# Performance work log

Hardware: AMD Instinct MI355X
Metric: run time of the kernel (lower is better)

The kernel has to match this reference:

```python
import jax, jax.numpy as jnp
import numpy as np
from jax import lax

B, N, E = 256, 100_000, 3_200_000
VOCAB, EMB, FT, DIM, OUT = 65, 128, 41, 32, 128
BN_EPS = 1e-5


def setup_inputs() -> dict:
    key = jax.random.key(0)
    ks = jax.random.split(key, 40)
    f = lambda i, shape: jax.random.normal(ks[i], shape, jnp.float32) * 0.05
    inp = {
        'xd': jax.random.randint(ks[0], (B, 100), 0, VOCAB),
        'xt': jax.random.normal(ks[1], (N, FT), jnp.float32),
        'edge_index': jax.random.randint(ks[2], (2, E), 0, N),
        'batch': jnp.sort(jax.random.randint(ks[3], (N,), 0, B)),
        'y': jax.random.normal(ks[4], (B,), jnp.float32),
        # drug branch params
        'emb': f(5, (VOCAB, EMB)),
        'conv_w': f(6, (32, 100, 8)),   # OIH for Conv1d(100->32, k=8)
        'conv_b': f(7, (32,)),
        'fcd_w': f(8, (32 * 121, OUT)),
        'fcd_b': f(9, (OUT,)),
        # GIN layer 1 MLP (41->32->32)
        'g1_w1': f(10, (FT, DIM)), 'g1_b1': f(11, (DIM,)),
        'g1_w2': f(12, (DIM, DIM)), 'g1_b2': f(13, (DIM,)),
        # GIN layers 2-5 MLPs (32->32->32), stacked
        'gw1': f(14, (4, DIM, DIM)), 'gb1': f(15, (4, DIM)),
        'gw2': f(16, (4, DIM, DIM)), 'gb2': f(17, (4, DIM)),
        # BatchNorm (eval mode running stats) for 5 layers
        'bn_g': f(18, (5, DIM)) + 1.0,
        'bn_b': f(19, (5, DIM)),
        'bn_rm': f(20, (5, DIM)),
        'bn_rv': jax.random.uniform(ks[21], (5, DIM), jnp.float32, 0.5, 1.5),
        # protein fc + classifier
        'fct_w': f(22, (DIM, OUT)), 'fct_b': f(23, (OUT,)),
        'c1_w': f(24, (256, 1024)), 'c1_b': f(25, (1024,)),
        'c2_w': f(26, (1024, 256)), 'c2_b': f(27, (256,)),
        'c3_w': f(28, (256, 1)), 'c3_b': f(29, (1,)),
    }
    return inp


def reference(xd, xt, edge_index, batch, y, emb, conv_w, conv_b, fcd_w, fcd_b,
              g1_w1, g1_b1, g1_w2, g1_b2, gw1, gb1, gw2, gb2,
              bn_g, bn_b, bn_rm, bn_rv, fct_w, fct_b,
              c1_w, c1_b, c2_w, c2_b, c3_w, c3_b):
    # ---- drug branch ----
    e = emb[xd]                                        # [B, 100, 128]
    c = lax.conv_general_dilated(e, conv_w, (1,), 'VALID',
                                 dimension_numbers=('NCH', 'OIH', 'NCH'))
    c = c + conv_b[None, :, None]                      # [B, 32, 121]
    xd_f = c.reshape(B, 32 * 121) @ fcd_w + fcd_b      # [B, 128]

    src, dst = edge_index[0], edge_index[1]
    h = xt
    for i in range(5):
        agg = h + jax.ops.segment_sum(h[src], dst, num_segments=N)
        if i == 0:
            w1, b1, w2, b2 = g1_w1, g1_b1, g1_w2, g1_b2
        else:
            w1, b1, w2, b2 = gw1[i - 1], gb1[i - 1], gw2[i - 1], gb2[i - 1]
        h = jax.nn.relu(agg @ w1 + b1) @ w2 + b2       # GIN MLP
        h = jax.nn.relu(h)                              # F.relu after conv
        h = bn_g[i] * (h - bn_rm[i]) * lax.rsqrt(bn_rv[i] + BN_EPS) + bn_b[i]
    pooled = jax.ops.segment_sum(h, batch, num_segments=B)  # global_add_pool
    xt_f = jax.nn.relu(pooled @ fct_w + fct_b)         # dropout = identity (eval)

    # ---- classifier ----
    xj = jnp.concatenate([xd_f, xt_f], axis=1)         # [B, 256]
    h1 = jax.nn.relu(xj @ c1_w + c1_b)
    h2 = jax.nn.relu(h1 @ c2_w + c2_b)
    out = (h2 @ c3_w + c3_b).squeeze(1)                # [B]
    return out, y
```

## Files before the change

### kernel.cpp

```cpp
#include <hip/hip_runtime.h>

typedef unsigned int u32;
typedef unsigned char u8;

#define NN 100000
#define NE 3200000
#define NB 256
#define FTD 41
#define DIM 32
#define NBK 782
#define SCHUNK 8000

typedef __fp16 fp16x2 __attribute__((ext_vector_type(2)));

__device__ __forceinline__ float h16f(u32 bits) {
  union { unsigned short s; _Float16 h; } c;
  c.s = (unsigned short)bits;
  return (float)c.h;
}
__device__ __forceinline__ u32 pk2(float a, float b) {
  union { fp16x2 h; u32 u; } c;
  c.h = __builtin_amdgcn_cvt_pkrtz(a, b);
  return c.u;
}

__device__ __forceinline__ u8 f8enc(float v) {
  union { _Float16 h; unsigned short u; } cv;
  cv.h = (_Float16)(v * 0.00390625f);
  u32 h = cv.u;
  u32 mag = h & 0x7fffu;
  u32 base = mag >> 7;
  u32 low = mag & 0x7fu;
  base += (low > 0x40u || (low == 0x40u && (base & 1u))) ? 1u : 0u;
  if (base > 0x7eu) base = 0x7eu;
  return (u8)(((h >> 8) & 0x80u) | base);
}

__device__ __forceinline__ void acc4(u32 w, float* a) {
#pragma unroll
  for (int i = 0; i < 4; i++) {
    u32 bb = (w >> (8 * i)) & 0xffu;
    a[i] += h16f(((bb & 0x80u) << 8) | ((bb & 0x7fu) << 7));
  }
}
__device__ __forceinline__ void accrow(uint4 r0, uint4 r1, float* acc) {
  acc4(r0.x, acc + 0);  acc4(r0.y, acc + 4);
  acc4(r0.z, acc + 8);  acc4(r0.w, acc + 12);
  acc4(r1.x, acc + 16); acc4(r1.y, acc + 20);
  acc4(r1.z, acc + 24); acc4(r1.w, acc + 28);
}

__global__ __launch_bounds__(256) void k_bzero(int* __restrict__ bcnt) {
  int g = blockIdx.x * 256 + threadIdx.x;
  if (g < NBK) bcnt[g] = 0;
}

__global__ __launch_bounds__(256) void k_bhist(const int* __restrict__ ei,
                                               int* __restrict__ bcnt) {
  __shared__ int h[NBK];
  int t = threadIdx.x;
  for (int i = t; i < NBK; i += 256) h[i] = 0;
  __syncthreads();
  for (int g = blockIdx.x * 256 + t; g < NE; g += gridDim.x * 256)
    atomicAdd(&h[ei[NE + g] >> 7], 1);
  __syncthreads();
  for (int i = t; i < NBK; i += 256)
    if (h[i]) atomicAdd(&bcnt[i], h[i]);
}

__global__ __launch_bounds__(1024) void k_bscan(const int* __restrict__ bcnt,
                                                int* __restrict__ boff,
                                                int* __restrict__ bcur) {
  __shared__ int sm[1024];
  int t = threadIdx.x;
  int v = (t < NBK) ? bcnt[t] : 0;
  sm[t] = v;
  __syncthreads();
  for (int d = 1; d < 1024; d <<= 1) {
    int x = (t >= d) ? sm[t - d] : 0;
    __syncthreads();
    sm[t] += x;
    __syncthreads();
  }
  if (t < NBK) {
    int excl = sm[t] - v;
    boff[t] = excl;
    bcur[t] = excl;
  }
  if (t == 0) boff[NBK] = NE;
}

__global__ __launch_bounds__(256) void k_bscatter(const int* __restrict__ ei,
                                                  int* __restrict__ bcur,
                                                  int* __restrict__ ppack) {
  __shared__ int lexcl[NBK];
  __shared__ int lcur[NBK];
  __shared__ int gdelta[NBK];
  __shared__ int lbuf[SCHUNK];
  __shared__ unsigned short lbkt[SCHUNK];
  __shared__ int sm[256];
  int t = threadIdx.x;
  int e0 = blockIdx.x * SCHUNK;
  for (int i = t; i < NBK; i += 256) lexcl[i] = 0;
  __syncthreads();
  for (int i = t; i < SCHUNK; i += 256)
    atomicAdd(&lexcl[((u32)ei[NE + e0 + i]) >> 7], 1);
  __syncthreads();
  int b0 = t * 4;
  int c0 = 0, c1 = 0, c2 = 0, c3 = 0;
  if (b0 < NBK) {
    c0 = lexcl[b0];
    c1 = (b0 + 1 < NBK) ? lexcl[b0 + 1] : 0;
    c2 = (b0 + 2 < NBK) ? lexcl[b0 + 2] : 0;
    c3 = (b0 + 3 < NBK) ? lexcl[b0 + 3] : 0;
  }
  int tot = c0 + c1 + c2 + c3;
  sm[t] = tot;
  __syncthreads();
  for (int d = 1; d < 256; d <<= 1) {
    int x = (t >= d) ? sm[t - d] : 0;
    __syncthreads();
    sm[t] += x;
    __syncthreads();
  }
  int base = sm[t] - tot;
  if (b0 < NBK) {
    int cnts[4] = {c0, c1, c2, c3};
    int e = base;
#pragma unroll
    for (int j = 0; j < 4; j++) {
      int b = b0 + j;
      if (b < NBK) {
        int c = cnts[j];
        lexcl[b] = e;
        lcur[b] = e;
        if (c > 0) gdelta[b] = atomicAdd(&bcur[b], c) - e;
        e += c;
      }
    }
  }
  __syncthreads();
  for (int i = t; i < SCHUNK; i += 256) {
    int s = ei[e0 + i];
    u32 d = (u32)ei[NE + e0 + i];
    int b = d >> 7;
    int p = atomicAdd(&lcur[b], 1);
    lbuf[p] = (int)(((d & 127u) << 20) | (u32)s);
    lbkt[p] = (unsigned short)b;
  }
  __syncthreads();
  for (int i = t; i < SCHUNK; i += 256) {
    int b = lbkt[i];
    ppack[gdelta[b] + i] = lbuf[i];
  }
}

__global__ __launch_bounds__(256) void k_bfinal(const int* __restrict__ boff,
                                                const int* __restrict__ ppack,
                                                int* __restrict__ off,
                                                int* __restrict__ srcs) {
  __shared__ int ncnt[128];
  __shared__ int nincl[128];
  int b = blockIdx.x, t = threadIdx.x;
  int e0 = boff[b], e1 = boff[b + 1];
  if (t < 128) ncnt[t] = 0;
  __syncthreads();
  for (int i = e0 + t; i < e1; i += 256) atomicAdd(&ncnt[((u32)ppack[i]) >> 20], 1);
  __syncthreads();
  if (t < 128) nincl[t] = ncnt[t];
  __syncthreads();
  for (int d = 1; d < 128; d <<= 1) {
    int x = 0;
    if (t < 128 && t >= d) x = nincl[t - d];
    __syncthreads();
    if (t < 128) nincl[t] += x;
    __syncthreads();
  }
  int node0 = b * 128;
  if (t < 128) {
    int excl = nincl[t] - ncnt[t];
    int node = node0 + t;
    if (node < NN) off[node] = e0 + excl;
    ncnt[t] = excl;
  }
  if (b == 0 && t == 0) off[NN] = NE;
  __syncthreads();
  for (int i = e0 + t; i < e1; i += 256) {
    u32 v = (u32)ppack[i];
    int dl = v >> 20;
    int pos = atomicAdd(&ncnt[dl], 1);
    srcs[e0 + pos] = (int)(v & 0xFFFFF);
  }
}

__global__ __launch_bounds__(256) void k_conv(
    const int* __restrict__ xd, const float* __restrict__ emb,
    const float* __restrict__ convw, const float* __restrict__ convb,
    float* __restrict__ C) {
  __shared__ float e_s[100 * 129 + 12];
  __shared__ float w_s[4 * 800];
  __shared__ int xd_s[100];
  int t = threadIdx.x;
  int b = blockIdx.x >> 3;
  int og = (blockIdx.x & 7) << 2;
  if (t < 100) xd_s[t] = xd[b * 100 + t];
  __syncthreads();
  for (int i = t; i < 12800; i += 256)
    e_s[(i >> 7) * 129 + (i & 127)] = emb[xd_s[i >> 7] * 128 + (i & 127)];
  for (int i = t; i < 3200; i += 256) w_s[i] = convw[og * 800 + i];
  __syncthreads();
  int ol = t >> 6;
  int ht = t & 63;
  int h0 = ht * 2;
  float a0 = 0.f, a1 = 0.f;
  const float4* wv = (const float4*)&w_s[ol * 800];
  for (int i = 0; i < 100; i++) {
    const float* ep = &e_s[i * 129 + h0];
    float e0 = ep[0], e1 = ep[1], e2 = ep[2], e3 = ep[3], e4 = ep[4];
    float e5 = ep[5], e6 = ep[6], e7 = ep[7], e8 = ep[8];
    float4 wa = wv[i * 2], wb = wv[i * 2 + 1];
    a0 += e0 * wa.x + e1 * wa.y + e2 * wa.z + e3 * wa.w +
          e4 * wb.x + e5 * wb.y + e6 * wb.z + e7 * wb.w;
    a1 += e1 * wa.x + e2 * wa.y + e3 * wa.z + e4 * wa.w +
          e5 * wb.x + e6 * wb.y + e7 * wb.z + e8 * wb.w;
  }
  int o = og + ol;
  float bb = convb[o];
  float* cp = &C[b * 3872 + o * 121];
  if (h0 < 121) cp[h0] = a0 + bb;
  if (h0 + 1 < 121) cp[h0 + 1] = a1 + bb;
}

__global__ __launch_bounds__(256) void k_fcd(
    const float* __restrict__ C, const float* __restrict__ fcdw,
    const float* __restrict__ fcdb, float* __restrict__ XJ) {
  __shared__ float c_s[3872];
  __shared__ float red[128];
  int t = threadIdx.x, b = blockIdx.x;
  for (int i = t; i < 3872; i += 256) c_s[i] = C[b * 3872 + i];
  __syncthreads();
  int j = t & 127, half = t >> 7;
  float acc = 0.f;
  int k0 = half * 1936;
  for (int k = k0; k < k0 + 1936; k++) acc += c_s[k] * fcdw[k * 128 + j];
  if (half) red[j] = acc;
  __syncthreads();
  if (!half) XJ[b * 256 + j] = acc + red[j] + fcdb[j];
}

__global__ __launch_bounds__(256) void k_z1(
    const float* __restrict__ xt, const float* __restrict__ w1,
    u8* __restrict__ Z, float* __restrict__ pool) {
  __shared__ float xs[256 * FTD];
  __shared__ float w1s[FTD * DIM];
  int t = threadIdx.x;
  int base = blockIdx.x * 256;
  int g = base + t;
  if (g < NB * DIM) pool[g] = 0.f;
  for (int i = t; i < FTD * DIM; i += 256) w1s[i] = w1[i];
  int cnt = min(256, NN - base);
  for (int i = t; i < cnt * FTD; i += 256) xs[i] = xt[base * FTD + i];
  __syncthreads();
  int n = base + t;
  if (n < NN) {
    float acc[DIM];
#pragma unroll
    for (int j = 0; j < DIM; j++) acc[j] = 0.f;
    for (int k = 0; k < FTD; k++) {
      float xk = xs[t * FTD + k];
#pragma unroll
      for (int j = 0; j < DIM; j++) acc[j] += xk * w1s[k * DIM + j];
    }
    u8* zp = &Z[n * DIM];
#pragma unroll
    for (int j = 0; j < DIM; j++) zp[j] = f8enc(acc[j]);
  }
}

template <int HAS_NEXT, int DO_POOL>
__global__ __launch_bounds__(256) void k_gin(
    const int* __restrict__ off, const int* __restrict__ srcs,
    const u8* __restrict__ Zin, const float* __restrict__ b1,
    const float* __restrict__ w2, const float* __restrict__ b2,
    const float* __restrict__ bng, const float* __restrict__ bnb,
    const float* __restrict__ bnrm, const float* __restrict__ bnrv,
    const float* __restrict__ w1n, u8* __restrict__ Zout,
    float* __restrict__ pool, const int* __restrict__ batch) {
  __shared__ float w2s[DIM * DIM];
  __shared__ float w1ns[DIM * DIM];
  __shared__ u32 aggs[256 * 17];
  int t = threadIdx.x;
  for (int i = t; i < DIM * DIM; i += 256) {
    w2s[i] = w2[i];
    if (HAS_NEXT) w1ns[i] = w1n[i];
  }
  int m = t >> 2, p = t & 3;
  int n = blockIdx.x * 64 + m;
  if (n < NN) {
    float acc[DIM];
#pragma unroll
    for (int i = 0; i < DIM; i++) acc[i] = 0.f;
    int beg = off[n], end = off[n + 1];
    if (p == 0) {
      const uint4* zr = (const uint4*)(Zin + n * DIM);
      uint4 r0 = zr[0], r1 = zr[1];
      accrow(r0, r1, acc);
    }
    int j = beg + p;
    for (; j + 4 < end; j += 8) {
      int sA = srcs[j], sB = srcs[j + 4];
      const uint4* ra = (const uint4*)(Zin + sA * DIM);
      const uint4* rb = (const uint4*)(Zin + sB * DIM);
      uint4 a0 = ra[0], a1 = ra[1];
      uint4 c0 = rb[0], c1 = rb[1];
      accrow(a0, a1, acc);
      accrow(c0, c1, acc);
    }
    if (j < end) {
      int sA = srcs[j];
      const uint4* ra = (const uint4*)(Zin + sA * DIM);
      uint4 a0 = ra[0], a1 = ra[1];
      accrow(a0, a1, acc);
    }
#pragma unroll
    for (int q = 0; q < 16; q++)
      aggs[t * 17 + q] = pk2(acc[2 * q], acc[2 * q + 1]);
  }
  __syncthreads();
  int g = t >> 5, f = t & 31;
  float b1f = b1[f], b2f = b2[f];
  float sc = bng[f] * rsqrtf(bnrv[f] + 1e-5f);
  float sh = bnb[f] - bnrm[f] * sc;
  int w = f >> 1, hi = f & 1;
#pragma unroll 1
  for (int mm = 0; mm < 8; mm++) {
    int lm = g * 8 + mm;
    int node = blockIdx.x * 64 + lm;
    if (node >= NN) break;
    int s4 = lm * 4;
    u32 u0 = aggs[(s4 + 0) * 17 + w];
    u32 u1 = aggs[(s4 + 1) * 17 + w];
    u32 u2 = aggs[(s4 + 2) * 17 + w];
    u32 u3 = aggs[(s4 + 3) * 17 + w];
    float agg = (h16f(hi ? (u0 >> 16) : (u0 & 0xffffu)) +
                 h16f(hi ? (u1 >> 16) : (u1 & 0xffffu))) +
                (h16f(hi ? (u2 >> 16) : (u2 & 0xffffu)) +
                 h16f(hi ? (u3 >> 16) : (u3 & 0xffffu)));
    agg *= 256.0f;
    float hid = fmaxf(agg + b1f, 0.f);
    float o = b2f;
#pragma unroll
    for (int k = 0; k < DIM; k++) o += __shfl(hid, k, 32) * w2s[k * DIM + f];
    float hn = fmaxf(o, 0.f) * sc + sh;
    if (HAS_NEXT) {
      float z = 0.f;
#pragma unroll
      for (int k = 0; k < DIM; k++) z += __shfl(hn, k, 32) * w1ns[k * DIM + f];
      Zout[node * DIM + f] = f8enc(z);
    }
    if (DO_POOL) atomicAdd(&pool[batch[node] * DIM + f], hn);
  }
}

__global__ __launch_bounds__(128) void k_fct(
    const float* __restrict__ pool, const float* __restrict__ fctw,
    const float* __restrict__ fctb, float* __restrict__ XJ) {
  __shared__ float p_s[DIM];
  int t = threadIdx.x, b = blockIdx.x;
  if (t < DIM) p_s[t] = pool[b * DIM + t];
  __syncthreads();
  float acc = fctb[t];
  for (int k = 0; k < DIM; k++) acc += p_s[k] * fctw[k * 128 + t];
  XJ[b * 256 + 128 + t] = fmaxf(acc, 0.f);
}

__global__ __launch_bounds__(256) void k_c1(
    const float* __restrict__ XJ, const float* __restrict__ w,
    const float* __restrict__ bias, float* __restrict__ H1) {
  __shared__ float xs[256];
  int t = threadIdx.x, b = blockIdx.y;
  xs[t] = XJ[b * 256 + t];
  __syncthreads();
  int j = blockIdx.x * 256 + t;
  float acc = bias[j];
  for (int k = 0; k < 256; k++) acc += xs[k] * w[k * 1024 + j];
  H1[b * 1024 + j] = fmaxf(acc, 0.f);
}

__global__ __launch_bounds__(256) void k_c2(
    const float* __restrict__ H1, const float* __restrict__ w,
    const float* __restrict__ bias, float* __restrict__ H2) {
  __shared__ float hs[1024];
  int t = threadIdx.x, b = blockIdx.x;
  for (int i = t; i < 1024; i += 256) hs[i] = H1[b * 1024 + i];
  __syncthreads();
  float acc = bias[t];
  for (int k = 0; k < 1024; k++) acc += hs[k] * w[k * 256 + t];
  H2[b * 256 + t] = fmaxf(acc, 0.f);
}

__global__ __launch_bounds__(64) void k_c3(
    const float* __restrict__ H2, const float* __restrict__ w,
    const float* __restrict__ bias, const float* __restrict__ y,
    float* __restrict__ out) {
  int b = blockIdx.x * 64 + threadIdx.x;
  float acc = bias[0];
  for (int k = 0; k < 256; k++) acc += H2[b * 256 + k] * w[k];
  out[b] = acc;
  out[NB + b] = y[b];
}

extern "C" void kernel_launch(void* const* d_in, const int* in_sizes, int n_in,
                              void* d_out, int out_size, void* d_ws,
                              size_t ws_size, hipStream_t stream) {
  const int* xd = (const int*)d_in[0];
  const float* xt = (const float*)d_in[1];
  const int* ei = (const int*)d_in[2];
  const int* batch = (const int*)d_in[3];
  const float* y = (const float*)d_in[4];
  const float* emb = (const float*)d_in[5];
  const float* convw = (const float*)d_in[6];
  const float* convb = (const float*)d_in[7];
  const float* fcdw = (const float*)d_in[8];
  const float* fcdb = (const float*)d_in[9];
  const float* g1w1 = (const float*)d_in[10];
  const float* g1b1 = (const float*)d_in[11];
  const float* g1w2 = (const float*)d_in[12];
  const float* g1b2 = (const float*)d_in[13];
  const float* gw1 = (const float*)d_in[14];
  const float* gb1 = (const float*)d_in[15];
  const float* gw2 = (const float*)d_in[16];
  const float* gb2 = (const float*)d_in[17];
  const float* bng = (const float*)d_in[18];
  const float* bnb = (const float*)d_in[19];
  const float* bnrm = (const float*)d_in[20];
  const float* bnrv = (const float*)d_in[21];
  const float* fctw = (const float*)d_in[22];
  const float* fctb = (const float*)d_in[23];
  const float* c1w = (const float*)d_in[24];
  const float* c1b = (const float*)d_in[25];
  const float* c2w = (const float*)d_in[26];
  const float* c2b = (const float*)d_in[27];
  const float* c3w = (const float*)d_in[28];
  const float* c3b = (const float*)d_in[29];
  float* out = (float*)d_out;

  u8* Z0 = (u8*)d_ws;
  u8* Z1 = Z0 + (size_t)NN * DIM;
  int* srcs = (int*)(Z1 + (size_t)NN * DIM);
  int* off = srcs + NE;
  int* bcnt = off + NN + 1;
  int* boff = bcnt + NBK;
  int* bcur = boff + NBK + 1;
  int* ppack = bcur + NBK;
  float* C = (float*)ppack;
  float* XJ = C + (size_t)NB * 3872;
  float* H1 = XJ + NB * 256;
  float* H2 = H1 + NB * 1024;
  float* POOL = H2 + NB * 256;

  int nblk = (NN + 255) / 256;
  int gblk = (NN + 63) / 64;

  k_bzero<<<(NBK + 255) / 256, 256, 0, stream>>>(bcnt);
  k_bhist<<<512, 256, 0, stream>>>(ei, bcnt);
  k_bscan<<<1, 1024, 0, stream>>>(bcnt, boff, bcur);
  k_bscatter<<<NE / SCHUNK, 256, 0, stream>>>(ei, bcur, ppack);
  k_bfinal<<<NBK, 256, 0, stream>>>(boff, ppack, off, srcs);

  k_conv<<<NB * 8, 256, 0, stream>>>(xd, emb, convw, convb, C);
  k_fcd<<<NB, 256, 0, stream>>>(C, fcdw, fcdb, XJ);

  k_z1<<<nblk, 256, 0, stream>>>(xt, g1w1, Z0, POOL);
  u8* zin = Z0;
  u8* zout = Z1;
  for (int i = 0; i < 5; i++) {
    const float *b1, *w2, *b2;
    if (i == 0) { b1 = g1b1; w2 = g1w2; b2 = g1b2; }
    else {
      b1 = gb1 + (i - 1) * DIM;
      w2 = gw2 + (i - 1) * DIM * DIM;
      b2 = gb2 + (i - 1) * DIM;
    }
    const float* w1n = gw1 + i * DIM * DIM;
    if (i < 4)
      k_gin<1, 0><<<gblk, 256, 0, stream>>>(
          off, srcs, zin, b1, w2, b2, bng + i * DIM, bnb + i * DIM,
          bnrm + i * DIM, bnrv + i * DIM, w1n, zout, POOL, batch);
    else
      k_gin<0, 1><<<gblk, 256, 0, stream>>>(
          off, srcs, zin, b1, w2, b2, bng + i * DIM, bnb + i * DIM,
          bnrm + i * DIM, bnrv + i * DIM, w1n, zout, POOL, batch);
    u8* tmp = zin; zin = zout; zout = tmp;
  }
  k_fct<<<NB, 128, 0, stream>>>(POOL, fctw, fctb, XJ);
  k_c1<<<dim3(4, NB), 256, 0, stream>>>(XJ, c1w, c1b, H1);
  k_c2<<<NB, 256, 0, stream>>>(H1, c2w, c2b, H2);
  k_c3<<<4, 64, 0, stream>>>(H2, c3w, c3b, y, out);
}
```

Baseline: 731.6 us.

## Use eight threads per node in GIN gather and chunk conv embedding staging

The GIN aggregation kernel now assigns eight threads per node, with 32 nodes per block instead of 64. This doubles gather parallelism per node to hide memory latency on high-degree rows, and the bounds checks are dropped because NN divides evenly by 32. The drug conv kernel stages the embedding in two 50-channel chunks with a padded stride of 132 and reads float2 vectors, which cuts shared memory use and may allow more blocks per CU. The trade-offs are double the GIN block count and an extra barrier per conv chunk.

Result: faster. 685.7 us (-6.3%).

```diff
diff --git a/kernel.cpp b/kernel.cpp
--- a/kernel.cpp
+++ b/kernel.cpp
@@ -197,32 +197,36 @@
     const int* __restrict__ xd, const float* __restrict__ emb,
     const float* __restrict__ convw, const float* __restrict__ convb,
     float* __restrict__ C) {
-  __shared__ float e_s[100 * 129 + 12];
+  __shared__ float e_s[50 * 132 + 16];
   __shared__ float w_s[4 * 800];
   __shared__ int xd_s[100];
   int t = threadIdx.x;
   int b = blockIdx.x >> 3;
   int og = (blockIdx.x & 7) << 2;
   if (t < 100) xd_s[t] = xd[b * 100 + t];
-  __syncthreads();
-  for (int i = t; i < 12800; i += 256)
-    e_s[(i >> 7) * 129 + (i & 127)] = emb[xd_s[i >> 7] * 128 + (i & 127)];
   for (int i = t; i < 3200; i += 256) w_s[i] = convw[og * 800 + i];
-  __syncthreads();
   int ol = t >> 6;
   int ht = t & 63;
   int h0 = ht * 2;
   float a0 = 0.f, a1 = 0.f;
   const float4* wv = (const float4*)&w_s[ol * 800];
-  for (int i = 0; i < 100; i++) {
-    const float* ep = &e_s[i * 129 + h0];
-    float e0 = ep[0], e1 = ep[1], e2 = ep[2], e3 = ep[3], e4 = ep[4];
-    float e5 = ep[5], e6 = ep[6], e7 = ep[7], e8 = ep[8];
-    float4 wa = wv[i * 2], wb = wv[i * 2 + 1];
-    a0 += e0 * wa.x + e1 * wa.y + e2 * wa.z + e3 * wa.w +
-          e4 * wb.x + e5 * wb.y + e6 * wb.z + e7 * wb.w;
-    a1 += e1 * wa.x + e2 * wa.y + e3 * wa.z + e4 * wa.w +
-          e5 * wb.x + e6 * wb.y + e7 * wb.z + e8 * wb.w;
+  for (int c = 0; c < 2; c++) {
+    __syncthreads();
+    for (int idx = t; idx < 6400; idx += 256) {
+      int ch = idx >> 7, pos = idx & 127;
+      e_s[ch * 132 + pos] = emb[xd_s[c * 50 + ch] * 128 + pos];
+    }
+    __syncthreads();
+    for (int i = 0; i < 50; i++) {
+      const float2* ep2 = (const float2*)&e_s[i * 132 + h0];
+      float2 v0 = ep2[0], v1 = ep2[1], v2 = ep2[2], v3 = ep2[3], v4 = ep2[4];
+      int ci = c * 50 + i;
+      float4 wa = wv[ci * 2], wb = wv[ci * 2 + 1];
+      a0 += v0.x * wa.x + v0.y * wa.y + v1.x * wa.z + v1.y * wa.w +
+            v2.x * wb.x + v2.y * wb.y + v3.x * wb.z + v3.y * wb.w;
+      a1 += v0.y * wa.x + v1.x * wa.y + v1.y * wa.z + v2.x * wa.w +
+            v2.y * wb.x + v3.x * wb.y + v3.y * wb.z + v4.x * wb.w;
+    }
   }
   int o = og + ol;
   float bb = convb[o];
@@ -294,9 +298,9 @@
     w2s[i] = w2[i];
     if (HAS_NEXT) w1ns[i] = w1n[i];
   }
-  int m = t >> 2, p = t & 3;
-  int n = blockIdx.x * 64 + m;
-  if (n < NN) {
+  int m = t >> 3, p = t & 7;
+  int n = blockIdx.x * 32 + m;
+  {
     float acc[DIM];
 #pragma unroll
     for (int i = 0; i < DIM; i++) acc[i] = 0.f;
@@ -307,8 +311,8 @@
       accrow(r0, r1, acc);
     }
     int j = beg + p;
-    for (; j + 4 < end; j += 8) {
-      int sA = srcs[j], sB = srcs[j + 4];
+    for (; j + 8 < end; j += 16) {
+      int sA = srcs[j], sB = srcs[j + 8];
       const uint4* ra = (const uint4*)(Zin + sA * DIM);
       const uint4* rb = (const uint4*)(Zin + sB * DIM);
       uint4 a0 = ra[0], a1 = ra[1];
@@ -333,19 +337,16 @@
   float sh = bnb[f] - bnrm[f] * sc;
   int w = f >> 1, hi = f & 1;
 #pragma unroll 1
-  for (int mm = 0; mm < 8; mm++) {
-    int lm = g * 8 + mm;
-    int node = blockIdx.x * 64 + lm;
-    if (node >= NN) break;
-    int s4 = lm * 4;
-    u32 u0 = aggs[(s4 + 0) * 17 + w];
-    u32 u1 = aggs[(s4 + 1) * 17 + w];
-    u32 u2 = aggs[(s4 + 2) * 17 + w];
-    u32 u3 = aggs[(s4 + 3) * 17 + w];
-    float agg = (h16f(hi ? (u0 >> 16) : (u0 & 0xffffu)) +
-                 h16f(hi ? (u1 >> 16) : (u1 & 0xffffu))) +
-                (h16f(hi ? (u2 >> 16) : (u2 & 0xffffu)) +
-                 h16f(hi ? (u3 >> 16) : (u3 & 0xffffu)));
+  for (int mm = 0; mm < 4; mm++) {
+    int lm = g * 4 + mm;
+    int node = blockIdx.x * 32 + lm;
+    int s8 = lm * 8;
+    float agg = 0.f;
+#pragma unroll
+    for (int q = 0; q < 8; q++) {
+      u32 u = aggs[(s8 + q) * 17 + w];
+      agg += h16f(hi ? (u >> 16) : (u & 0xffffu));
+    }
     agg *= 256.0f;
     float hid = fmaxf(agg + b1f, 0.f);
     float o = b2f;
@@ -460,7 +461,7 @@
   float* POOL = H2 + NB * 256;
 
   int nblk = (NN + 255) / 256;
-  int gblk = (NN + 63) / 64;
+  int gblk = NN / 32;
 
   k_bzero<<<(NBK + 255) / 256, 256, 0, stream>>>(bcnt);
   k_bhist<<<512, 256, 0, stream>>>(ei, bcnt);
```
